# Performance work log

Hardware: AMD Instinct MI355X
Metric: run time of the kernel (lower is better)

## Reference

```python
import jax, jax.numpy as jnp
import numpy as np

B, N, K = 4, 2048, 32
H, DS, DE = 128, 128, 128
NUM_IN = DS + DE + H  # 384
SCALE = 30.0
EPS = 1e-5


def setup_inputs() -> dict:
    key = jax.random.key(0)
    ks = jax.random.split(key, 9)
    s = 0.05
    return {
        "h_S": jax.random.normal(ks[0], (B, N, DS), jnp.float32),
        "h_V": jax.random.normal(ks[1], (B, N, H), jnp.float32),
        "h_E": jax.random.normal(ks[2], (B, N, K, DE), jnp.float32),
        "E_idx": jax.random.randint(ks[3], (B, N, K), 0, N, jnp.int64),
        "mask_attend": jnp.ones((B, N, K), jnp.float32),
        "W1_w": jax.random.normal(ks[4], (H + NUM_IN, H), jnp.float32) * s,
        "W1_b": jnp.zeros((H,), jnp.float32),
        "W2_w": jax.random.normal(ks[5], (H, H), jnp.float32) * s,
        "W2_b": jnp.zeros((H,), jnp.float32),
        "ln_g": jnp.ones((H,), jnp.float32),
        "ln_b": jnp.zeros((H,), jnp.float32),
    }


def gather_nodes(nodes, idx):
    # nodes: [B, N, D], idx: [B, N, K] -> [B, N, K, D]
    b, n, k = idx.shape
    d = nodes.shape[-1]
    flat = jnp.broadcast_to(idx.reshape(b, n * k, 1), (b, n * k, d))
    return jnp.take_along_axis(nodes, flat, axis=1).reshape(b, n, k, d)


def layer_norm(x, g, b):
    mu = jnp.mean(x, axis=-1, keepdims=True)
    var = jnp.var(x, axis=-1, keepdims=True)
    return (x - mu) * jax.lax.rsqrt(var + EPS) * g + b


def reference(h_S, h_V, h_E, E_idx, mask_attend, W1_w, W1_b, W2_w, W2_b, ln_g, ln_b):
    # h_ES = cat(h_E, gather(h_S))  -> [B,N,K,DE+DS]
    h_ES = jnp.concatenate([h_E, gather_nodes(h_S, E_idx)], axis=-1)
    # h_EXV = cat(h_ES, gather(h_V)) -> [B,N,K,DE+DS+H], masked
    h_EXV = jnp.concatenate([h_ES, gather_nodes(h_V, E_idx)], axis=-1)
    h_EXV = mask_attend[..., None] * h_EXV
    # h_EV = cat(h_V expanded, h_EXV) -> [B,N,K,H+NUM_IN]
    h_V_exp = jnp.broadcast_to(h_V[:, :, None, :], (h_V.shape[0], h_V.shape[1], K, h_V.shape[2]))
    h_EV = jnp.concatenate([h_V_exp, h_EXV], axis=-1)
    # per-edge 2-layer MLP (exact GELU as torch.nn.GELU)
    h = jax.nn.gelu(jnp.einsum("bnkf,fh->bnkh", h_EV, W1_w) + W1_b, approximate=False)
    h_message = jnp.einsum("bnkh,hg->bnkg", h, W2_w) + W2_b
    dh = jnp.sum(h_message, axis=-2) / SCALE
    # dropout is identity in eval mode
    return layer_norm(h_V + dh, ln_g, ln_b)
```

## Files before the change

### kernel.cpp

```cpp
#include <hip/hip_runtime.h>
#include <math.h>

typedef float f32x4 __attribute__((ext_vector_type(4)));
typedef short s16x8 __attribute__((ext_vector_type(8)));
typedef unsigned u32x4 __attribute__((ext_vector_type(4)));

#define N_NODES 2048
#define KEDGE 32
#define HDIM 128
#define SB() __builtin_amdgcn_sched_barrier(0)

__device__ __forceinline__ short f2bf(float f){
  unsigned u = __builtin_bit_cast(unsigned, f);
  u += 0x7fffu + ((u >> 16) & 1u);
  return (short)(u >> 16);
}
__device__ __forceinline__ float bf2f(short s){
  unsigned u = ((unsigned)(unsigned short)s) << 16;
  return __builtin_bit_cast(float, u);
}
__device__ __forceinline__ unsigned cvt_pk_bf16(float a, float b){
  unsigned r;
  asm("v_cvt_pk_bf16_f32 %0, %1, %2" : "=v"(r) : "v"(a), "v"(b));
  return r;
}
__device__ __forceinline__ float fast_gelu(float x){
  float t = x * (-2.3022078f - 0.1029527f * x * x);
  float e = __builtin_amdgcn_exp2f(t);
  return x * __builtin_amdgcn_rcpf(1.0f + e);
}
__device__ __forceinline__ void gld16(const void* g, void* l){
  __builtin_amdgcn_global_load_lds(
      (const __attribute__((address_space(1))) void*)g,
      (__attribute__((address_space(3))) void*)l, 16, 0, 0);
}
__device__ __forceinline__ f32x4 mfma16(s16x8 a, s16x8 b, f32x4 c){
  return __builtin_amdgcn_mfma_f32_16x16x32_bf16(a, b, c, 0, 0, 0);
}

__global__ void prep1(const float* __restrict__ W1, const float* __restrict__ W2,
                      short* __restrict__ W1f, short* __restrict__ W2f,
                      unsigned* __restrict__ flag){
  if (blockIdx.x == 320){
    if (threadIdx.x == 0) *flag = 0u;
    return;
  }
  int t = blockIdx.x * 256 + threadIdx.x;
  if (t < 65536){
    int ks = t >> 12, r = t & 4095;
    int ct = r >> 9;  r &= 511;
    int lane = r >> 3, j = r & 7;
    int k = ks*32 + (lane>>4)*8 + j;
    int n = ct*16 + (lane&15);
    W1f[t] = f2bf(W1[k*128 + n]);
  } else if (t < 81920){
    int t2 = t - 65536;
    int ks = t2 >> 12, r = t2 & 4095;
    int ct = r >> 9;  r &= 511;
    int lane = r >> 3, j = r & 7;
    int k = ks*32 + (lane>>4)*8 + j;
    int n = ct*16 + (lane&15);
    W2f[t2] = f2bf(W2[k*128 + n]);
  }
}

__global__ __launch_bounds__(256)
void prep2(const float* __restrict__ hS, const float* __restrict__ hV,
           const float* __restrict__ b1, const short* __restrict__ W1f,
           short* __restrict__ Zb, unsigned* __restrict__ UHb,
           const unsigned* __restrict__ Ei_u, unsigned* __restrict__ flag){
  if (blockIdx.x >= 128){
    int t = ((int)blockIdx.x - 128)*256 + threadIdx.x;
    unsigned v = Ei_u[2*t + 1];
    unsigned long long m = __ballot(v != 0u);
    if ((threadIdx.x & 63) == 0 && m) atomicOr(flag, 1u);
    return;
  }
  const int tid = threadIdx.x;
  const int w = tid >> 6, lane = tid & 63, l15 = lane & 15, lg = lane >> 4;
  const int nb = ((int)blockIdx.x*4 + w)*16;

  f32x4 accz[8], accu[8];
  #pragma unroll
  for (int ct = 0; ct < 8; ++ct){ accz[ct] = (f32x4){0,0,0,0}; accu[ct] = (f32x4){0,0,0,0}; }

  #pragma unroll
  for (int ks = 0; ks < 4; ++ks){
    const float* p = hS + (long)(nb + l15)*128 + ks*32 + lg*8;
    float4 x = *(const float4*)p, y = *(const float4*)(p + 4);
    u32x4 pk;
    pk[0] = cvt_pk_bf16(x.x, x.y); pk[1] = cvt_pk_bf16(x.z, x.w);
    pk[2] = cvt_pk_bf16(y.x, y.y); pk[3] = cvt_pk_bf16(y.z, y.w);
    s16x8 a = __builtin_bit_cast(s16x8, pk);
    #pragma unroll
    for (int ct = 0; ct < 8; ++ct){
      s16x8 bf = *(const s16x8*)(W1f + (8+ks)*4096 + ct*512 + lane*8);
      accz[ct] = mfma16(a, bf, accz[ct]);
    }
  }
  #pragma unroll
  for (int ks = 0; ks < 4; ++ks){
    const float* p = hV + (long)(nb + l15)*128 + ks*32 + lg*8;
    float4 x = *(const float4*)p, y = *(const float4*)(p + 4);
    u32x4 pk;
    pk[0] = cvt_pk_bf16(x.x, x.y); pk[1] = cvt_pk_bf16(x.z, x.w);
    pk[2] = cvt_pk_bf16(y.x, y.y); pk[3] = cvt_pk_bf16(y.z, y.w);
    s16x8 a = __builtin_bit_cast(s16x8, pk);
    #pragma unroll
    for (int ct = 0; ct < 8; ++ct){
      s16x8 bfd = *(const s16x8*)(W1f + (12+ks)*4096 + ct*512 + lane*8);
      accz[ct] = mfma16(a, bfd, accz[ct]);
      s16x8 bfa = *(const s16x8*)(W1f + (0+ks)*4096 + ct*512 + lane*8);
      accu[ct] = mfma16(a, bfa, accu[ct]);
    }
  }

  float b1v[8];
  #pragma unroll
  for (int ct = 0; ct < 8; ++ct) b1v[ct] = b1[ct*16 + l15];

  #pragma unroll
  for (int ct = 0; ct < 8; ++ct)
    #pragma unroll
    for (int i = 0; i < 4; ++i){
      const long row = nb + lg*4 + i;
      Zb[row*128 + ct*16 + l15] = f2bf(accz[ct][i]);
      unsigned u16 = (unsigned)(unsigned short)f2bf(accu[ct][i] + b1v[ct]);
      unsigned h16 = (unsigned)(unsigned short)f2bf(hV[row*128 + ct*16 + l15]);
      UHb[row*128 + l15*8 + ct] = u16 | (h16 << 16);
    }
}

__global__ __launch_bounds__(256, 1)
void fusedF(const float* __restrict__ hE, const int* __restrict__ Eidx,
            const float* __restrict__ mask, const short* __restrict__ W1f,
            const short* __restrict__ W2f, const short* __restrict__ Zb,
            const unsigned* __restrict__ UHb, const unsigned* __restrict__ idx_flag,
            const float* __restrict__ W2b, const float* __restrict__ lng,
            const float* __restrict__ lnb, float* __restrict__ out)
{
  __shared__ __align__(16) char smem[34816];

  const int tid  = threadIdx.x;
  const int w    = tid >> 6;
  const int team = w >> 1;
  const int half = w & 1;
  const int ctb  = half * 4;
  const int lane = tid & 63;
  const int l15  = lane & 15;
  const int lg   = lane >> 4;

  const int bid  = (int)blockIdx.x;
  const int bswz = (bid & 7)*128 + (bid >> 3);
  const int n0 = (bswz*2 + team) * 4;
  const long zrow0 = (long)(n0 >> 11) * N_NODES;
  char* mybuf  = smem + team*16384;
  short* vpark = (short*)(smem + 32768 + team*1024);

  const int rr = lane >> 5;
  const unsigned t0 = (unsigned)((rr << 9) | (((lane & 31) << 4) ^ (rr << 4)));

  s16x8 wf[4][4];
  #pragma unroll
  for (int ks = 0; ks < 4; ++ks)
    #pragma unroll
    for (int c = 0; c < 4; ++c)
      wf[ks][c] = *(const s16x8*)(W1f + (4+ks)*4096 + (ctb+c)*512 + lane*8);
  SB();

  s16x8 ifr[2];
  #pragma unroll
  for (int c2 = 0; c2 < 2; ++c2){
    const int active = ((lg >> 1) == c2);
    const int j = l15 - 8*(lg & 1);
    s16x8 f;
    #pragma unroll
    for (int e = 0; e < 8; ++e)
      f[e] = (active && j == e) ? (short)0x3F80 : (short)0;
    ifr[c2] = f;
  }

  const int is64 = (*idx_flag == 0u) ? 1 : 0;

  int e0, eZ;
  {
    const int ea = n0*32 + l15;
    const int eb = n0*32 + 16 + l15;
    e0 = Eidx[ea << is64];
    eZ = Eidx[eb << is64];
  }
  float maskC = mask[n0*32 + l15];
  s16x8 uhC = *(const s16x8*)((const short*)UHb + (long)n0*256 + l15*16 + ctb*2);
  SB();
  #pragma unroll
  for (int j = 0; j < 4; ++j){
    const int qq = half*4 + j;
    const unsigned off = (unsigned)(qq*1024) | (t0 ^ (unsigned)((2*qq & 6) << 4));
    gld16((const char*)hE + (size_t)n0*16384 + off, mybuf + qq*1024);
  }
  SB();
  s16x8 zbC[2];
  #pragma unroll
  for (int kk = 0; kk < 2; ++kk)
    zbC[kk] = *(const s16x8*)(Zb + (zrow0 + e0)*128 + (half*2+kk)*32 + lg*8);
  SB();
  asm volatile("s_waitcnt vmcnt(0)" ::: "memory");
  SB();
  __builtin_amdgcn_s_barrier();

  float vacc[4];
  #pragma unroll
  for (int c = 0; c < 4; ++c) vacc[c] = 0.f;

  #pragma unroll
  for (int t = 0; t < 8; ++t){
    const int tn = t + 1;
    float maskN = 0.f; s16x8 uhN{}; int eN = 0;
    s16x8 zbN0{}, zbN1{};
    if (t < 7){
      const int nn_n = n0 + (tn >> 1);
      SB();
      maskN = mask[nn_n*32 + (tn&1)*16 + l15];
      uhN = *(const s16x8*)((const short*)UHb + (long)nn_n*256 + l15*16 + ctb*2);
      {
        const int t2 = t + 2;
        const int nz = (t2 <= 7) ? (n0 + (t2>>1)) : n0;
        const int hz = (t2 <= 7) ? (t2&1) : 0;
        eN = Eidx[(nz*32 + hz*16 + l15) << is64];
      }
      SB();
      {
        const size_t eb = (size_t)nn_n*16384 + (size_t)(tn&1)*8192;
        char* sbuf = mybuf + (tn&1)*8192;
        #pragma unroll
        for (int j = 0; j < 4; ++j){
          const int qq = half*4 + j;
          const unsigned off = (unsigned)(qq*1024) | (t0 ^ (unsigned)((2*qq & 6) << 4));
          gld16((const char*)hE + eb + off, sbuf + qq*1024);
        }
      }
      SB();
      zbN0 = *(const s16x8*)(Zb + (zrow0 + eZ)*128 + (half*2+0)*32 + lg*8);
      zbN1 = *(const s16x8*)(Zb + (zrow0 + eZ)*128 + (half*2+1)*32 + lg*8);
      SB();
      asm volatile("s_waitcnt vmcnt(11)" ::: "memory");
      SB();
    } else {
      asm volatile("s_waitcnt vmcnt(0)" ::: "memory");
      SB();
    }
    __builtin_amdgcn_s_barrier();

    __builtin_amdgcn_s_setprio(1);

    f32x4 acc1[4];
    #pragma unroll
    for (int c = 0; c < 4; ++c) acc1[c] = (f32x4){0,0,0,0};

    const char* cbuf = mybuf + (t&1)*8192;
    const int sw = (l15 & 7) << 4;
    const int rowb = l15 * 512;
    #pragma unroll
    for (int ks = 0; ks < 4; ++ks){
      const int c0 = ks*128 + lg*32;
      float4 ex = *(const float4*)(cbuf + rowb + (c0 ^ sw));
      float4 ey = *(const float4*)(cbuf + rowb + ((c0 + 16) ^ sw));
      u32x4 pk;
      pk[0] = cvt_pk_bf16(ex.x, ex.y); pk[1] = cvt_pk_bf16(ex.z, ex.w);
      pk[2] = cvt_pk_bf16(ey.x, ey.y); pk[3] = cvt_pk_bf16(ey.z, ey.w);
      s16x8 a = __builtin_bit_cast(s16x8, pk);
      #pragma unroll
      for (int c = 0; c < 4; ++c)
        acc1[c] = mfma16(a, wf[ks][c], acc1[c]);
    }

    if (t < 7){
      asm volatile("s_waitcnt vmcnt(9)" ::: "memory");
      SB();
    }

    #pragma unroll
    for (int kk = 0; kk < 2; ++kk)
      #pragma unroll
      for (int c2 = 0; c2 < 2; ++c2)
        acc1[kk*2 + c2] = mfma16(zbC[kk], ifr[c2], acc1[kk*2 + c2]);

    float uv[4];
    #pragma unroll
    for (int c = 0; c < 4; ++c) uv[c] = bf2f(uhC[2*c]);
    float mi[4];
    #pragma unroll
    for (int i = 0; i < 4; ++i) mi[i] = __shfl(maskC, lg*4 + i, 64);
    #pragma unroll
    for (int c = 0; c < 4; ++c)
      #pragma unroll
      for (int i = 0; i < 4; ++i)
        vacc[c] += fast_gelu(uv[c] + mi[i]*acc1[c][i]);

    __builtin_amdgcn_s_setprio(0);

    if (t & 1){
      short* vl = vpark + (t >> 1)*128;
      #pragma unroll
      for (int c = 0; c < 4; ++c){
        float s = vacc[c];
        s += __shfl_xor(s, 16, 64);
        s += __shfl_xor(s, 32, 64);
        vacc[c] = 0.f;
        if (lg == c)
          vl[(ctb + c)*16 + l15] = f2bf(s);
      }
    }

    if (t < 7){
      maskC = maskN; uhC = uhN; eZ = eN;
      zbC[0] = zbN0; zbC[1] = zbN1;
    }
  }

  asm volatile("s_waitcnt lgkmcnt(0)" ::: "memory");
  SB();
  __builtin_amdgcn_s_barrier();

  float w2b8[8], lngv[2], lnbv[2];
  #pragma unroll
  for (int ct = 0; ct < 8; ++ct) w2b8[ct] = W2b[ct*16 + l15];
  #pragma unroll
  for (int q = 0; q < 2; ++q){
    const int c = (lg*2 + q)*16 + l15;
    lngv[q] = lng[c]; lnbv[q] = lnb[c];
  }

  #pragma unroll
  for (int j = 0; j < 2; ++j){
    const int nd = half*2 + j;
    const short* vl = vpark + nd*128;
    f32x4 acc2[8];
    #pragma unroll
    for (int ct = 0; ct < 8; ++ct) acc2[ct] = (f32x4){0,0,0,0};
    #pragma unroll
    for (int ks2 = 0; ks2 < 4; ++ks2){
      s16x8 av = *(const s16x8*)(vl + ks2*32 + lg*8);
      const short* wb2 = W2f + ks2*4096 + lane*8;
      #pragma unroll
      for (int ct = 0; ct < 8; ++ct){
        s16x8 bf = *(const s16x8*)(wb2 + ct*512);
        acc2[ct] = mfma16(av, bf, acc2[ct]);
      }
    }

    s16x8 uh0 = *(const s16x8*)((const short*)UHb + (long)(n0+nd)*256 + l15*16);
    s16x8 uh1 = *(const s16x8*)((const short*)UHb + (long)(n0+nd)*256 + l15*16 + 8);
    float hv[8];
    #pragma unroll
    for (int c = 0; c < 4; ++c){ hv[c] = bf2f(uh0[2*c+1]); hv[4+c] = bf2f(uh1[2*c+1]); }

    float res[8], vs = 0.f, vq = 0.f;
    #pragma unroll
    for (int ct = 0; ct < 8; ++ct){
      float dh  = (acc2[ct][0] + 32.0f * w2b8[ct]) * (1.0f/30.0f);
      float val = hv[ct] + dh;
      res[ct] = val;
      vs += val; vq += val*val;
    }
    vs += __shfl_xor(vs, 1, 64);  vs += __shfl_xor(vs, 2, 64);
    vs += __shfl_xor(vs, 4, 64);  vs += __shfl_xor(vs, 8, 64);
    vq += __shfl_xor(vq, 1, 64);  vq += __shfl_xor(vq, 2, 64);
    vq += __shfl_xor(vq, 4, 64);  vq += __shfl_xor(vq, 8, 64);
    const float mu  = vs * (1.0f/128.0f);
    const float var = vq * (1.0f/128.0f) - mu*mu;
    const float rs  = rsqrtf(var + 1e-5f);

    const long nodeoff = (long)(n0 + nd) * HDIM;
    #pragma unroll
    for (int q = 0; q < 2; ++q){
      const int ct = lg*2 + q;
      out[nodeoff + ct*16 + l15] = (res[ct] - mu) * rs * lngv[q] + lnbv[q];
    }
  }
}

extern "C" void kernel_launch(void* const* d_in, const int* in_sizes, int n_in,
                              void* d_out, int out_size, void* d_ws, size_t ws_size,
                              hipStream_t stream) {
  const float* hS  = (const float*)d_in[0];
  const float* hV  = (const float*)d_in[1];
  const float* hE  = (const float*)d_in[2];
  const int*   Ei  = (const int*)d_in[3];
  const float* mk  = (const float*)d_in[4];
  const float* W1w = (const float*)d_in[5];
  const float* W1b = (const float*)d_in[6];
  const float* W2w = (const float*)d_in[7];
  const float* W2b = (const float*)d_in[8];
  const float* lng = (const float*)d_in[9];
  const float* lnb = (const float*)d_in[10];

  short* W1f = (short*)d_ws;
  short* W2f = W1f + 65536;
  unsigned* flag = (unsigned*)((char*)d_ws + 163840);
  short* Zb = (short*)((char*)d_ws + 164096);
  unsigned* UHb = (unsigned*)((char*)d_ws + 2261248);

  prep1<<<321, 256, 0, stream>>>(W1w, W2w, W1f, W2f, flag);
  prep2<<<640, 256, 0, stream>>>(hS, hV, W1b, W1f, Zb, UHb, (const unsigned*)Ei, flag);
  fusedF<<<1024, 256, 0, stream>>>(hE, Ei, mk, W1f, W2f, Zb, UHb, flag,
                                   W2b, lng, lnb, (float*)d_out);
}
```

Baseline: 81.36 us.

## Split node groups across all four waves to double block count and halve LDS

Each block now handles one 4-node group with all four waves splitting the 128 output columns two tiles each, instead of two teams of two waves each handling a node group. The grid doubles to 2048 blocks and LDS per block halves, which lowers per-wave register use (fewer W1 fragments and accumulators) and may allow more resident blocks per CU. In exchange each block issues smaller hE loads per wave and the per-block fixed costs (W1 fragment loads, index setup, epilogue W2 reads) are paid twice as often. The vmcnt wait counts are retuned to match the fewer outstanding loads per wave.

New measurement: 84.53 us (median of 3 runs). 1.04x slower.

```diff
diff --git a/kernel.cpp b/kernel.cpp
--- a/kernel.cpp
+++ b/kernel.cpp
@@ -3,6 +3,7 @@
 
 typedef float f32x4 __attribute__((ext_vector_type(4)));
 typedef short s16x8 __attribute__((ext_vector_type(8)));
+typedef short s16x4 __attribute__((ext_vector_type(4)));
 typedef unsigned u32x4 __attribute__((ext_vector_type(4)));
 
 #define N_NODES 2048
@@ -139,32 +140,30 @@
             const float* __restrict__ W2b, const float* __restrict__ lng,
             const float* __restrict__ lnb, float* __restrict__ out)
 {
-  __shared__ __align__(16) char smem[34816];
+  __shared__ __align__(16) char smem[17408];
 
   const int tid  = threadIdx.x;
   const int w    = tid >> 6;
-  const int team = w >> 1;
-  const int half = w & 1;
-  const int ctb  = half * 4;
+  const int ctb  = w * 2;
   const int lane = tid & 63;
   const int l15  = lane & 15;
   const int lg   = lane >> 4;
 
   const int bid  = (int)blockIdx.x;
-  const int bswz = (bid & 7)*128 + (bid >> 3);
-  const int n0 = (bswz*2 + team) * 4;
+  const int bswz = (bid & 7)*256 + (bid >> 3);
+  const int n0 = bswz * 4;
   const long zrow0 = (long)(n0 >> 11) * N_NODES;
-  char* mybuf  = smem + team*16384;
-  short* vpark = (short*)(smem + 32768 + team*1024);
+  char* mybuf  = smem;
+  short* vpark = (short*)(smem + 16384);
 
   const int rr = lane >> 5;
   const unsigned t0 = (unsigned)((rr << 9) | (((lane & 31) << 4) ^ (rr << 4)));
 
-  s16x8 wf[4][4];
+  s16x8 wf[4][2];
   #pragma unroll
   for (int ks = 0; ks < 4; ++ks)
     #pragma unroll
-    for (int c = 0; c < 4; ++c)
+    for (int c = 0; c < 2; ++c)
       wf[ks][c] = *(const s16x8*)(W1f + (4+ks)*4096 + (ctb+c)*512 + lane*8);
   SB();
 
@@ -190,38 +189,33 @@
     eZ = Eidx[eb << is64];
   }
   float maskC = mask[n0*32 + l15];
-  s16x8 uhC = *(const s16x8*)((const short*)UHb + (long)n0*256 + l15*16 + ctb*2);
-  SB();
-  #pragma unroll
-  for (int j = 0; j < 4; ++j){
-    const int qq = half*4 + j;
+  s16x4 uhC = *(const s16x4*)((const short*)UHb + (long)n0*256 + l15*16 + ctb*2);
+  SB();
+  #pragma unroll
+  for (int j = 0; j < 2; ++j){
+    const int qq = w*2 + j;
     const unsigned off = (unsigned)(qq*1024) | (t0 ^ (unsigned)((2*qq & 6) << 4));
     gld16((const char*)hE + (size_t)n0*16384 + off, mybuf + qq*1024);
   }
   SB();
-  s16x8 zbC[2];
-  #pragma unroll
-  for (int kk = 0; kk < 2; ++kk)
-    zbC[kk] = *(const s16x8*)(Zb + (zrow0 + e0)*128 + (half*2+kk)*32 + lg*8);
+  s16x8 zbC = *(const s16x8*)(Zb + (zrow0 + e0)*128 + w*32 + lg*8);
   SB();
   asm volatile("s_waitcnt vmcnt(0)" ::: "memory");
   SB();
   __builtin_amdgcn_s_barrier();
 
-  float vacc[4];
-  #pragma unroll
-  for (int c = 0; c < 4; ++c) vacc[c] = 0.f;
+  float vacc[2] = {0.f, 0.f};
 
   #pragma unroll
   for (int t = 0; t < 8; ++t){
     const int tn = t + 1;
-    float maskN = 0.f; s16x8 uhN{}; int eN = 0;
-    s16x8 zbN0{}, zbN1{};
+    float maskN = 0.f; s16x4 uhN{}; int eN = 0;
+    s16x8 zbN{};
     if (t < 7){
       const int nn_n = n0 + (tn >> 1);
       SB();
       maskN = mask[nn_n*32 + (tn&1)*16 + l15];
-      uhN = *(const s16x8*)((const short*)UHb + (long)nn_n*256 + l15*16 + ctb*2);
+      uhN = *(const s16x4*)((const short*)UHb + (long)nn_n*256 + l15*16 + ctb*2);
       {
         const int t2 = t + 2;
         const int nz = (t2 <= 7) ? (n0 + (t2>>1)) : n0;
@@ -233,17 +227,16 @@
         const size_t eb = (size_t)nn_n*16384 + (size_t)(tn&1)*8192;
         char* sbuf = mybuf + (tn&1)*8192;
         #pragma unroll
-        for (int j = 0; j < 4; ++j){
-          const int qq = half*4 + j;
+        for (int j = 0; j < 2; ++j){
+          const int qq = w*2 + j;
           const unsigned off = (unsigned)(qq*1024) | (t0 ^ (unsigned)((2*qq & 6) << 4));
           gld16((const char*)hE + eb + off, sbuf + qq*1024);
         }
       }
       SB();
-      zbN0 = *(const s16x8*)(Zb + (zrow0 + eZ)*128 + (half*2+0)*32 + lg*8);
-      zbN1 = *(const s16x8*)(Zb + (zrow0 + eZ)*128 + (half*2+1)*32 + lg*8);
-      SB();
-      asm volatile("s_waitcnt vmcnt(11)" ::: "memory");
+      zbN = *(const s16x8*)(Zb + (zrow0 + eZ)*128 + w*32 + lg*8);
+      SB();
+      asm volatile("s_waitcnt vmcnt(7)" ::: "memory");
       SB();
     } else {
       asm volatile("s_waitcnt vmcnt(0)" ::: "memory");
@@ -253,9 +246,8 @@
 
     __builtin_amdgcn_s_setprio(1);
 
-    f32x4 acc1[4];
-    #pragma unroll
-    for (int c = 0; c < 4; ++c) acc1[c] = (f32x4){0,0,0,0};
+    f32x4 acc1[2];
+    acc1[0] = (f32x4){0,0,0,0}; acc1[1] = (f32x4){0,0,0,0};
 
     const char* cbuf = mybuf + (t&1)*8192;
     const int sw = (l15 & 7) << 4;
@@ -269,30 +261,26 @@
       pk[0] = cvt_pk_bf16(ex.x, ex.y); pk[1] = cvt_pk_bf16(ex.z, ex.w);
       pk[2] = cvt_pk_bf16(ey.x, ey.y); pk[3] = cvt_pk_bf16(ey.z, ey.w);
       s16x8 a = __builtin_bit_cast(s16x8, pk);
-      #pragma unroll
-      for (int c = 0; c < 4; ++c)
-        acc1[c] = mfma16(a, wf[ks][c], acc1[c]);
+      acc1[0] = mfma16(a, wf[ks][0], acc1[0]);
+      acc1[1] = mfma16(a, wf[ks][1], acc1[1]);
     }
 
     if (t < 7){
-      asm volatile("s_waitcnt vmcnt(9)" ::: "memory");
-      SB();
-    }
-
-    #pragma unroll
-    for (int kk = 0; kk < 2; ++kk)
-      #pragma unroll
-      for (int c2 = 0; c2 < 2; ++c2)
-        acc1[kk*2 + c2] = mfma16(zbC[kk], ifr[c2], acc1[kk*2 + c2]);
-
-    float uv[4];
-    #pragma unroll
-    for (int c = 0; c < 4; ++c) uv[c] = bf2f(uhC[2*c]);
+      asm volatile("s_waitcnt vmcnt(6)" ::: "memory");
+      SB();
+    }
+
+    #pragma unroll
+    for (int c2 = 0; c2 < 2; ++c2)
+      acc1[c2] = mfma16(zbC, ifr[c2], acc1[c2]);
+
+    float uv[2];
+    uv[0] = bf2f(uhC[0]); uv[1] = bf2f(uhC[2]);
     float mi[4];
     #pragma unroll
     for (int i = 0; i < 4; ++i) mi[i] = __shfl(maskC, lg*4 + i, 64);
     #pragma unroll
-    for (int c = 0; c < 4; ++c)
+    for (int c = 0; c < 2; ++c)
       #pragma unroll
       for (int i = 0; i < 4; ++i)
         vacc[c] += fast_gelu(uv[c] + mi[i]*acc1[c][i]);
@@ -302,7 +290,7 @@
     if (t & 1){
       short* vl = vpark + (t >> 1)*128;
       #pragma unroll
-      for (int c = 0; c < 4; ++c){
+      for (int c = 0; c < 2; ++c){
         float s = vacc[c];
         s += __shfl_xor(s, 16, 64);
         s += __shfl_xor(s, 32, 64);
@@ -313,8 +301,7 @@
     }
 
     if (t < 7){
-      maskC = maskN; uhC = uhN; eZ = eN;
-      zbC[0] = zbN0; zbC[1] = zbN1;
+      maskC = maskN; uhC = uhN; eZ = eN; zbC = zbN;
     }
   }
 
@@ -331,9 +318,8 @@
     lngv[q] = lng[c]; lnbv[q] = lnb[c];
   }
 
-  #pragma unroll
-  for (int j = 0; j < 2; ++j){
-    const int nd = half*2 + j;
+  {
+    const int nd = w;
     const short* vl = vpark + nd*128;
     f32x4 acc2[8];
     #pragma unroll
@@ -403,6 +389,6 @@
 
   prep1<<<321, 256, 0, stream>>>(W1w, W2w, W1f, W2f, flag);
   prep2<<<640, 256, 0, stream>>>(hS, hV, W1b, W1f, Zb, UHb, (const unsigned*)Ei, flag);
-  fusedF<<<1024, 256, 0, stream>>>(hE, Ei, mk, W1f, W2f, Zb, UHb, flag,
+  fusedF<<<2048, 256, 0, stream>>>(hE, Ei, mk, W1f, W2f, Zb, UHb, flag,
                                    W2b, lng, lnb, (float*)d_out);
 }
```
